# Kernel tuning notes

Measured on AMD Instinct MI355X. Metric: run time of the kernel, lower is better.

Reference implementation:

```python
import jax, jax.numpy as jnp
import numpy as np
import math

B, D = 32768, 64

def setup_inputs() -> dict:
    key = jax.random.key(0)
    k1, k2, k3 = jax.random.split(key, 3)
    x = jax.random.normal(k1, (B, D), dtype=jnp.float32)
    grad_H = jax.random.normal(k2, (B, D), dtype=jnp.float32)
    # kaiming-normal-like init: std = sqrt(2 / fan_in), fan_in = D+1
    weight = jax.random.normal(k3, (D + 1, D * D), dtype=jnp.float32) * np.float32(math.sqrt(2.0 / (D + 1)))
    return {"x": x, "grad_H": grad_H, "weight": weight}

def reference(x, grad_H, weight):
    b, d = x.shape
    x1 = jnp.concatenate([x, jnp.ones((b, 1), dtype=x.dtype)], axis=1)  # (B, D+1)
    M = (x1 @ weight).reshape(b, d, d)                                   # (B, D, D)
    R = jnp.einsum('bik,bjk->bij', M, M) / jnp.asarray(math.sqrt(d), x.dtype)  # M @ M^T
    return jnp.einsum('bd,bde->be', grad_H, R)                           # (B, D)
```

## Files before the change

### kernel.cpp

```cpp
#include <hip/hip_runtime.h>
#include <stdint.h>

typedef _Float16  f16;
typedef f16       f16x2  __attribute__((ext_vector_type(2)));
typedef f16       f16x8  __attribute__((ext_vector_type(8)));
typedef float     f32x16v __attribute__((ext_vector_type(16)));
typedef float     f32x4v  __attribute__((ext_vector_type(4)));
typedef uint32_t  u32x4v  __attribute__((ext_vector_type(4)));
typedef unsigned short u16;

__device__ __forceinline__ f32x16v mfma16h(u32x4v a, u32x4v b, f32x16v c) {
  return __builtin_amdgcn_mfma_f32_32x32x16_f16(
      __builtin_bit_cast(f16x8, a), __builtin_bit_cast(f16x8, b), c, 0, 0, 0);
}

__global__ __launch_bounds__(256) void prep_w(const float* __restrict__ W,
                                              u16* __restrict__ w1h,
                                              u16* __restrict__ w2h) {
  __shared__ float Wl[4096];
  const int jj = blockIdx.x;
  const int t  = threadIdx.x;
  for (int idx = t; idx < 4096; idx += 256) Wl[idx] = W[jj * 4096 + idx];
  __syncthreads();
  for (int p = t; p < 512; p += 256) {
    const int c2 = p >> 6, l = p & 63;
    const int ct = c2 >> 2, s = c2 & 3;
    const int rowA = ct * 32 + (l & 31);
    const int k0   = s * 16 + (l >> 5) * 8;
    u16 v1[8], v2[8];
    #pragma unroll
    for (int e = 0; e < 8; ++e) {
      v2[e] = __builtin_bit_cast(u16, (f16)Wl[rowA * 64 + k0 + e]);
      v1[e] = __builtin_bit_cast(u16, (f16)Wl[(k0 + e) * 64 + rowA]);
    }
    u32x4v pk1, pk2;
    #pragma unroll
    for (int q = 0; q < 4; ++q) {
      pk1[q] = (uint32_t)v1[2*q] | ((uint32_t)v1[2*q+1] << 16);
      pk2[q] = (uint32_t)v2[2*q] | ((uint32_t)v2[2*q+1] << 16);
    }
    *reinterpret_cast<u32x4v*>(w1h + jj * 4096 + p * 8) = pk1;
    *reinterpret_cast<u32x4v*>(w2h + jj * 4096 + p * 8) = pk2;
  }
}

__global__ __launch_bounds__(512, 2) void rquad_main(
    const float* __restrict__ x, const float* __restrict__ g,
    const u16* __restrict__ w1h, const u16* __restrict__ w2h,
    float* __restrict__ out) {
  __shared__ u16 stage[4][4 * 4096];
  __shared__ u16 x1b[128 * 66];

  const int t    = threadIdx.x;
  const int lane = t & 63;
  const int wv   = t >> 6;
  const int jq   = wv >> 2;
  const int p    = (wv >> 1) & 1;
  const int ct   = wv & 1;
  const int bl   = lane & 31;
  const int half = lane >> 5;
  const long base = (long)blockIdx.x * 128;
  const int r0 = p * 64 + bl;
  const int r1 = r0 + 32;

  for (int idx = t; idx < 128 * 64; idx += 512) {
    int s = idx >> 6, c = idx & 63;
    x1b[s * 66 + c] = __builtin_bit_cast(u16, (f16)x[(base + s) * 64 + c]);
  }
  if (t < 128) x1b[t * 66 + 64] = (u16)0x3C00;

  f16x2 z0[4][4], z1[4][4];
  #pragma unroll
  for (int s = 0; s < 4; ++s) {
    const float* gp0 = g + (base + r0) * 64 + s * 16 + half * 8;
    const float* gp1 = g + (base + r1) * 64 + s * 16 + half * 8;
    f32x4v a = *reinterpret_cast<const f32x4v*>(gp0);
    f32x4v b = *reinterpret_cast<const f32x4v*>(gp0 + 4);
    f32x4v c = *reinterpret_cast<const f32x4v*>(gp1);
    f32x4v d = *reinterpret_cast<const f32x4v*>(gp1 + 4);
    z0[s][0] = f16x2{(f16)a[0], (f16)a[1]}; z0[s][1] = f16x2{(f16)a[2], (f16)a[3]};
    z0[s][2] = f16x2{(f16)b[0], (f16)b[1]}; z0[s][3] = f16x2{(f16)b[2], (f16)b[3]};
    z1[s][0] = f16x2{(f16)c[0], (f16)c[1]}; z1[s][1] = f16x2{(f16)c[2], (f16)c[3]};
    z1[s][2] = f16x2{(f16)d[0], (f16)d[1]}; z1[s][3] = f16x2{(f16)d[2], (f16)d[3]};
  }

  f32x16v acc0, acc1;

  auto stage_chunk = [&](const u16* __restrict__ Wsrc, int stream, int ci) {
    if (ci > 8 || (stream == 1 && ci == 8)) return;
    if (jq != stream) return;
    const int j0 = (stream == 0) ? ci * 4 : 33 + ci * 4;
    const int nq = (stream == 0 && ci == 8) ? 8 : 32;
    const int buf = stream * 2 + (ci & 1);
    const int w4 = wv & 3;
    for (int q = w4; q < nq; q += 4) {
      const u16* src = Wsrc + (size_t)(j0 + (q >> 3)) * 4096 + (q & 7) * 512 + lane * 8;
      __builtin_amdgcn_global_load_lds(
          (const __attribute__((address_space(1))) void*)src,
          (__attribute__((address_space(3))) void*)(&stage[buf][q * 512]),
          16, 0, 0);
    }
  };

  auto compute_j = [&](int buf, int jl, int jglob) {
    const u16* sb = &stage[buf][jl * 4096 + ct * 2048];
    u32x4v B[4];
    #pragma unroll
    for (int s = 0; s < 4; ++s)
      B[s] = *reinterpret_cast<const u32x4v*>(sb + s * 512 + lane * 8);
    const f16 xh0 = __builtin_bit_cast(f16, x1b[r0 * 66 + jglob]);
    const f16 xh1 = __builtin_bit_cast(f16, x1b[r1 * 66 + jglob]);
    const f16x2 xx0 = f16x2{xh0, xh0}, xx1 = f16x2{xh1, xh1};
    #pragma unroll
    for (int s = 0; s < 4; ++s) {
      u32x4v a0, a1;
      #pragma unroll
      for (int q = 0; q < 4; ++q) {
        f16x2 p0 = xx0 * z0[s][q];
        f16x2 p1 = xx1 * z1[s][q];
        a0[q] = __builtin_bit_cast(uint32_t, p0);
        a1[q] = __builtin_bit_cast(uint32_t, p1);
      }
      acc0 = mfma16h(a0, B[s], acc0);
      acc1 = mfma16h(a1, B[s], acc1);
    }
  };

  auto run_pass = [&](const u16* __restrict__ Wsrc) {
    #pragma unroll
    for (int r = 0; r < 16; ++r) { acc0[r] = 0.0f; acc1[r] = 0.0f; }
    stage_chunk(Wsrc, 0, 0);
    stage_chunk(Wsrc, 1, 0);
    __syncthreads();
    for (int st = 0; st <= 8; ++st) {
      stage_chunk(Wsrc, 0, st + 1);
      stage_chunk(Wsrc, 1, st + 1);
      if (jq == 0) {
        const int buf = st & 1;
        if (st < 8) {
          #pragma unroll
          for (int jl = 0; jl < 4; ++jl) compute_j(buf, jl, st * 4 + jl);
        } else {
          compute_j(buf, 0, 32);
        }
      } else {
        if (st < 8) {
          const int buf = 2 + (st & 1);
          #pragma unroll
          for (int jl = 0; jl < 4; ++jl) compute_j(buf, jl, 33 + st * 4 + jl);
        }
      }
      __syncthreads();
    }
  };

  __syncthreads();

  run_pass(w1h);

  float* vl = reinterpret_cast<float*>(&stage[0][0]);
  if (jq == 0) {
    #pragma unroll
    for (int r = 0; r < 16; ++r) {
      const int rr = (r & 3) + 8 * (r >> 2) + 4 * half;
      vl[(p * 64 + rr) * 68 + ct * 32 + bl]      = acc0[r];
      vl[(p * 64 + 32 + rr) * 68 + ct * 32 + bl] = acc1[r];
    }
  }
  __syncthreads();
  if (jq == 1) {
    #pragma unroll
    for (int r = 0; r < 16; ++r) {
      const int rr = (r & 3) + 8 * (r >> 2) + 4 * half;
      vl[(p * 64 + rr) * 68 + ct * 32 + bl]      += acc0[r];
      vl[(p * 64 + 32 + rr) * 68 + ct * 32 + bl] += acc1[r];
    }
  }
  __syncthreads();
  #pragma unroll
  for (int s = 0; s < 4; ++s) {
    const float* vp0 = &vl[r0 * 68 + s * 16 + half * 8];
    const float* vp1 = &vl[r1 * 68 + s * 16 + half * 8];
    f32x4v a = *reinterpret_cast<const f32x4v*>(vp0);
    f32x4v b = *reinterpret_cast<const f32x4v*>(vp0 + 4);
    f32x4v c = *reinterpret_cast<const f32x4v*>(vp1);
    f32x4v d = *reinterpret_cast<const f32x4v*>(vp1 + 4);
    z0[s][0] = f16x2{(f16)a[0], (f16)a[1]}; z0[s][1] = f16x2{(f16)a[2], (f16)a[3]};
    z0[s][2] = f16x2{(f16)b[0], (f16)b[1]}; z0[s][3] = f16x2{(f16)b[2], (f16)b[3]};
    z1[s][0] = f16x2{(f16)c[0], (f16)c[1]}; z1[s][1] = f16x2{(f16)c[2], (f16)c[3]};
    z1[s][2] = f16x2{(f16)d[0], (f16)d[1]}; z1[s][3] = f16x2{(f16)d[2], (f16)d[3]};
  }
  __syncthreads();

  run_pass(w2h);

  if (jq == 0) {
    #pragma unroll
    for (int r = 0; r < 16; ++r) {
      const int rr = (r & 3) + 8 * (r >> 2) + 4 * half;
      vl[(p * 64 + rr) * 68 + ct * 32 + bl]      = acc0[r];
      vl[(p * 64 + 32 + rr) * 68 + ct * 32 + bl] = acc1[r];
    }
  }
  __syncthreads();
  if (jq == 1) {
    #pragma unroll
    for (int r = 0; r < 16; ++r) {
      const int rr = (r & 3) + 8 * (r >> 2) + 4 * half;
      vl[(p * 64 + rr) * 68 + ct * 32 + bl]      += acc0[r];
      vl[(p * 64 + 32 + rr) * 68 + ct * 32 + bl] += acc1[r];
    }
  }
  __syncthreads();
  for (int idx = t; idx < 2048; idx += 512) {
    const int b = idx >> 4, c4 = (idx & 15) * 4;
    f32x4v v4 = *reinterpret_cast<const f32x4v*>(&vl[b * 68 + c4]);
    f32x4v o;
    o[0] = v4[0] * 0.125f; o[1] = v4[1] * 0.125f;
    o[2] = v4[2] * 0.125f; o[3] = v4[3] * 0.125f;
    *reinterpret_cast<f32x4v*>(out + (base + b) * 64 + c4) = o;
  }
}

extern "C" void kernel_launch(void* const* d_in, const int* in_sizes, int n_in,
                              void* d_out, int out_size, void* d_ws, size_t ws_size,
                              hipStream_t stream) {
  const float* x = (const float*)d_in[0];
  const float* g = (const float*)d_in[1];
  const float* W = (const float*)d_in[2];
  float* o = (float*)d_out;
  u16* w1h = (u16*)d_ws;
  u16* w2h = w1h + 65 * 4096;
  hipLaunchKernelGGL(prep_w, dim3(65), dim3(256), 0, stream, W, w1h, w2h);
  hipLaunchKernelGGL(rquad_main, dim3(256), dim3(512), 0, stream, x, g, w1h, w2h, o);
}
```

Measured before the change: 52.97 us.

## Stage half of W tiles in LDS, load other half directly; pack x into LDS

Only the first two k-slices of each W tile are staged through LDS via global_load_lds. The other two are read straight from global memory into registers inside compute_j, which halves the staging buffers. x is loaded with vector loads into a separate vl buffer and transposed into a packed pair-per-word x1p array, so each wave fetches both row scalars with one LDS read. This frees LDS and cuts staging traffic, but adds global-load latency on the compute path that the current pipeline does not hide.

```diff
diff --git a/kernel.cpp b/kernel.cpp
--- a/kernel.cpp
+++ b/kernel.cpp
@@ -22,8 +22,8 @@
   const int t  = threadIdx.x;
   for (int idx = t; idx < 4096; idx += 256) Wl[idx] = W[jj * 4096 + idx];
   __syncthreads();
-  for (int p = t; p < 512; p += 256) {
-    const int c2 = p >> 6, l = p & 63;
+  for (int pq = t; pq < 512; pq += 256) {
+    const int c2 = pq >> 6, l = pq & 63;
     const int ct = c2 >> 2, s = c2 & 3;
     const int rowA = ct * 32 + (l & 31);
     const int k0   = s * 16 + (l >> 5) * 8;
@@ -39,8 +39,8 @@
       pk1[q] = (uint32_t)v1[2*q] | ((uint32_t)v1[2*q+1] << 16);
       pk2[q] = (uint32_t)v2[2*q] | ((uint32_t)v2[2*q+1] << 16);
     }
-    *reinterpret_cast<u32x4v*>(w1h + jj * 4096 + p * 8) = pk1;
-    *reinterpret_cast<u32x4v*>(w2h + jj * 4096 + p * 8) = pk2;
+    *reinterpret_cast<u32x4v*>(w1h + jj * 4096 + pq * 8) = pk1;
+    *reinterpret_cast<u32x4v*>(w2h + jj * 4096 + pq * 8) = pk2;
   }
 }
 
@@ -48,8 +48,9 @@
     const float* __restrict__ x, const float* __restrict__ g,
     const u16* __restrict__ w1h, const u16* __restrict__ w2h,
     float* __restrict__ out) {
-  __shared__ u16 stage[4][4 * 4096];
-  __shared__ u16 x1b[128 * 66];
+  __shared__ u16      stage[4][8192];
+  __shared__ float    vl[128 * 68];
+  __shared__ uint32_t x1p[65 * 64];
 
   const int t    = threadIdx.x;
   const int lane = t & 63;
@@ -60,14 +61,26 @@
   const int bl   = lane & 31;
   const int half = lane >> 5;
   const long base = (long)blockIdx.x * 128;
-  const int r0 = p * 64 + bl;
-  const int r1 = r0 + 32;
-
-  for (int idx = t; idx < 128 * 64; idx += 512) {
-    int s = idx >> 6, c = idx & 63;
-    x1b[s * 66 + c] = __builtin_bit_cast(u16, (f16)x[(base + s) * 64 + c]);
-  }
-  if (t < 128) x1b[t * 66 + 64] = (u16)0x3C00;
+  const int r0 = p * 64 + bl, r1 = r0 + 32;
+
+  for (int q = t; q < 2048; q += 512) {
+    const int row = q >> 4, c4 = (q & 15) * 4;
+    *reinterpret_cast<f32x4v*>(&vl[row * 68 + c4]) =
+        *reinterpret_cast<const f32x4v*>(&x[(base + row) * 64 + c4]);
+  }
+  __syncthreads();
+  for (int idx = t; idx < 65 * 64; idx += 512) {
+    const int j = idx >> 6, q = idx & 63, pp = q >> 5, qq = q & 31;
+    uint32_t val;
+    if (j == 64) val = 0x3C003C00u;
+    else {
+      f16 a = (f16)vl[(pp * 64 + qq) * 68 + j];
+      f16 b = (f16)vl[(pp * 64 + 32 + qq) * 68 + j];
+      val = (uint32_t)__builtin_bit_cast(u16, a) |
+            ((uint32_t)__builtin_bit_cast(u16, b) << 16);
+    }
+    x1p[idx] = val;
+  }
 
   f16x2 z0[4][4], z1[4][4];
   #pragma unroll
@@ -78,87 +91,83 @@
     f32x4v b = *reinterpret_cast<const f32x4v*>(gp0 + 4);
     f32x4v c = *reinterpret_cast<const f32x4v*>(gp1);
     f32x4v d = *reinterpret_cast<const f32x4v*>(gp1 + 4);
-    z0[s][0] = f16x2{(f16)a[0], (f16)a[1]}; z0[s][1] = f16x2{(f16)a[2], (f16)a[3]};
-    z0[s][2] = f16x2{(f16)b[0], (f16)b[1]}; z0[s][3] = f16x2{(f16)b[2], (f16)b[3]};
-    z1[s][0] = f16x2{(f16)c[0], (f16)c[1]}; z1[s][1] = f16x2{(f16)c[2], (f16)c[3]};
-    z1[s][2] = f16x2{(f16)d[0], (f16)d[1]}; z1[s][3] = f16x2{(f16)d[2], (f16)d[3]};
+    z0[s][0] = f16x2{(f16)a[0],(f16)a[1]}; z0[s][1] = f16x2{(f16)a[2],(f16)a[3]};
+    z0[s][2] = f16x2{(f16)b[0],(f16)b[1]}; z0[s][3] = f16x2{(f16)b[2],(f16)b[3]};
+    z1[s][0] = f16x2{(f16)c[0],(f16)c[1]}; z1[s][1] = f16x2{(f16)c[2],(f16)c[3]};
+    z1[s][2] = f16x2{(f16)d[0],(f16)d[1]}; z1[s][3] = f16x2{(f16)d[2],(f16)d[3]};
   }
 
   f32x16v acc0, acc1;
 
-  auto stage_chunk = [&](const u16* __restrict__ Wsrc, int stream, int ci) {
-    if (ci > 8 || (stream == 1 && ci == 8)) return;
-    if (jq != stream) return;
-    const int j0 = (stream == 0) ? ci * 4 : 33 + ci * 4;
-    const int nq = (stream == 0 && ci == 8) ? 8 : 32;
-    const int buf = stream * 2 + (ci & 1);
-    const int w4 = wv & 3;
-    for (int q = w4; q < nq; q += 4) {
-      const u16* src = Wsrc + (size_t)(j0 + (q >> 3)) * 4096 + (q & 7) * 512 + lane * 8;
-      __builtin_amdgcn_global_load_lds(
-          (const __attribute__((address_space(1))) void*)src,
-          (__attribute__((address_space(3))) void*)(&stage[buf][q * 512]),
-          16, 0, 0);
+  auto stage_chunk = [&](const u16* __restrict__ Wsrc, int ci) {
+    const int nch = (jq == 0) ? 9 : 8;
+    if (ci >= nch) return;
+    const int j0  = (jq == 0) ? ci * 4 : 33 + ci * 4;
+    const int njs = (jq == 0 && ci == 8) ? 1 : 4;
+    const int buf = jq * 2 + (ci & 1);
+    #pragma unroll
+    for (int u = 0; u < 2; ++u) {
+      const int jl = 2 * p + u;
+      if (jl < njs) {
+        #pragma unroll
+        for (int s = 0; s < 2; ++s) {
+          const u16* src = Wsrc + (size_t)(j0 + jl) * 4096 + ct * 2048 + s * 512 + lane * 8;
+          __builtin_amdgcn_global_load_lds(
+              (const __attribute__((address_space(1))) void*)src,
+              (__attribute__((address_space(3))) void*)(
+                  &stage[buf][jl * 2048 + ct * 1024 + s * 512 + lane * 8]),
+              16, 0, 0);
+        }
+      }
     }
   };
 
-  auto compute_j = [&](int buf, int jl, int jglob) {
-    const u16* sb = &stage[buf][jl * 4096 + ct * 2048];
-    u32x4v B[4];
-    #pragma unroll
-    for (int s = 0; s < 4; ++s)
-      B[s] = *reinterpret_cast<const u32x4v*>(sb + s * 512 + lane * 8);
-    const f16 xh0 = __builtin_bit_cast(f16, x1b[r0 * 66 + jglob]);
-    const f16 xh1 = __builtin_bit_cast(f16, x1b[r1 * 66 + jglob]);
-    const f16x2 xx0 = f16x2{xh0, xh0}, xx1 = f16x2{xh1, xh1};
+  auto compute_j = [&](const u16* __restrict__ Wsrc, int buf, int jl, int jglob) {
+    const u16* gp = Wsrc + (size_t)jglob * 4096 + ct * 2048 + 1024 + lane * 8;
+    u32x4v B2 = *reinterpret_cast<const u32x4v*>(gp);
+    u32x4v B3 = *reinterpret_cast<const u32x4v*>(gp + 512);
+    const u16* sb = &stage[buf][jl * 2048 + ct * 1024 + lane * 8];
+    u32x4v B0 = *reinterpret_cast<const u32x4v*>(sb);
+    u32x4v B1 = *reinterpret_cast<const u32x4v*>(sb + 512);
+    const uint32_t xw = x1p[jglob * 64 + p * 32 + bl];
+    const f16 xlo = __builtin_bit_cast(f16, (u16)(xw & 0xffffu));
+    const f16 xhi = __builtin_bit_cast(f16, (u16)(xw >> 16));
+    const f16x2 xx0 = f16x2{xlo, xlo}, xx1 = f16x2{xhi, xhi};
+    u32x4v Bs[4] = {B0, B1, B2, B3};
     #pragma unroll
     for (int s = 0; s < 4; ++s) {
       u32x4v a0, a1;
       #pragma unroll
       for (int q = 0; q < 4; ++q) {
-        f16x2 p0 = xx0 * z0[s][q];
-        f16x2 p1 = xx1 * z1[s][q];
-        a0[q] = __builtin_bit_cast(uint32_t, p0);
-        a1[q] = __builtin_bit_cast(uint32_t, p1);
+        a0[q] = __builtin_bit_cast(uint32_t, f16x2(xx0 * z0[s][q]));
+        a1[q] = __builtin_bit_cast(uint32_t, f16x2(xx1 * z1[s][q]));
       }
-      acc0 = mfma16h(a0, B[s], acc0);
-      acc1 = mfma16h(a1, B[s], acc1);
+      acc0 = mfma16h(a0, Bs[s], acc0);
+      acc1 = mfma16h(a1, Bs[s], acc1);
     }
   };
 
   auto run_pass = [&](const u16* __restrict__ Wsrc) {
     #pragma unroll
     for (int r = 0; r < 16; ++r) { acc0[r] = 0.0f; acc1[r] = 0.0f; }
-    stage_chunk(Wsrc, 0, 0);
-    stage_chunk(Wsrc, 1, 0);
+    stage_chunk(Wsrc, 0);
     __syncthreads();
-    for (int st = 0; st <= 8; ++st) {
-      stage_chunk(Wsrc, 0, st + 1);
-      stage_chunk(Wsrc, 1, st + 1);
-      if (jq == 0) {
-        const int buf = st & 1;
-        if (st < 8) {
-          #pragma unroll
-          for (int jl = 0; jl < 4; ++jl) compute_j(buf, jl, st * 4 + jl);
-        } else {
-          compute_j(buf, 0, 32);
-        }
-      } else {
-        if (st < 8) {
-          const int buf = 2 + (st & 1);
-          #pragma unroll
-          for (int jl = 0; jl < 4; ++jl) compute_j(buf, jl, 33 + st * 4 + jl);
-        }
+    for (int st = 0; st < 9; ++st) {
+      stage_chunk(Wsrc, st + 1);
+      const int buf = jq * 2 + (st & 1);
+      if (st < 8) {
+        const int jbase = (jq == 0) ? st * 4 : 33 + st * 4;
+        #pragma unroll
+        for (int jl = 0; jl < 4; ++jl) compute_j(Wsrc, buf, jl, jbase + jl);
+      } else if (jq == 0) {
+        compute_j(Wsrc, buf, 0, 32);
       }
       __syncthreads();
     }
   };
 
-  __syncthreads();
-
   run_pass(w1h);
 
-  float* vl = reinterpret_cast<float*>(&stage[0][0]);
   if (jq == 0) {
     #pragma unroll
     for (int r = 0; r < 16; ++r) {
@@ -185,12 +194,11 @@
     f32x4v b = *reinterpret_cast<const f32x4v*>(vp0 + 4);
     f32x4v c = *reinterpret_cast<const f32x4v*>(vp1);
     f32x4v d = *reinterpret_cast<const f32x4v*>(vp1 + 4);
-    z0[s][0] = f16x2{(f16)a[0], (f16)a[1]}; z0[s][1] = f16x2{(f16)a[2], (f16)a[3]};
-    z0[s][2] = f16x2{(f16)b[0], (f16)b[1]}; z0[s][3] = f16x2{(f16)b[2], (f16)b[3]};
-    z1[s][0] = f16x2{(f16)c[0], (f16)c[1]}; z1[s][1] = f16x2{(f16)c[2], (f16)c[3]};
-    z1[s][2] = f16x2{(f16)d[0], (f16)d[1]}; z1[s][3] = f16x2{(f16)d[2], (f16)d[3]};
-  }
-  __syncthreads();
+    z0[s][0] = f16x2{(f16)a[0],(f16)a[1]}; z0[s][1] = f16x2{(f16)a[2],(f16)a[3]};
+    z0[s][2] = f16x2{(f16)b[0],(f16)b[1]}; z0[s][3] = f16x2{(f16)b[2],(f16)b[3]};
+    z1[s][0] = f16x2{(f16)c[0],(f16)c[1]}; z1[s][1] = f16x2{(f16)c[2],(f16)c[3]};
+    z1[s][2] = f16x2{(f16)d[0],(f16)d[1]}; z1[s][3] = f16x2{(f16)d[2],(f16)d[3]};
+  }
 
   run_pass(w2h);
 
@@ -212,13 +220,13 @@
     }
   }
   __syncthreads();
-  for (int idx = t; idx < 2048; idx += 512) {
-    const int b = idx >> 4, c4 = (idx & 15) * 4;
-    f32x4v v4 = *reinterpret_cast<const f32x4v*>(&vl[b * 68 + c4]);
+  for (int q = t; q < 2048; q += 512) {
+    const int row = q >> 4, c4 = (q & 15) * 4;
+    f32x4v v4 = *reinterpret_cast<const f32x4v*>(&vl[row * 68 + c4]);
     f32x4v o;
     o[0] = v4[0] * 0.125f; o[1] = v4[1] * 0.125f;
     o[2] = v4[2] * 0.125f; o[3] = v4[3] * 0.125f;
-    *reinterpret_cast<f32x4v*>(out + (base + b) * 64 + c4) = o;
+    *reinterpret_cast<f32x4v*>(&out[(base + row) * 64 + c4]) = o;
   }
 }
 
```

Measured after the change: 52.31 us. About the same (-1.3%).
